# Optimization experiments

Measured on AMD Instinct MI355X. Metric: run time of the kernel, lower is better.

The kernel has to match this reference:

```python
import jax, jax.numpy as jnp
import numpy as np
from jax import lax

K = 3          # kernel size
PAD = 1        # (K-1)//2
CIN = 256
COUT = 64
NSPLIT = CIN // COUT  # 4
EPS = 1e-5


def _conv2d(x, w, b):
    # x [B,C,H,W], w [O,I,K,K], b [O]
    y = lax.conv_general_dilated(x, w, (1, 1), [(PAD, PAD), (PAD, PAD)],
                                 dimension_numbers=("NCHW", "OIHW", "NCHW"))
    return y + b[None, :, None, None]


def _bilinear_sample(img, py, px):
    # img [C,H,W]; py,px [K2,H,W] absolute sample coords; zero outside borders
    H, W = img.shape[1], img.shape[2]
    y0 = jnp.floor(py)
    x0 = jnp.floor(px)
    wy1 = py - y0
    wx1 = px - x0
    wy0 = 1.0 - wy1
    wx0 = 1.0 - wx1

    def gather(yc, xc):
        valid = (yc >= 0) & (yc <= H - 1) & (xc >= 0) & (xc <= W - 1)
        yi = jnp.clip(yc, 0, H - 1).astype(jnp.int32)
        xi = jnp.clip(xc, 0, W - 1).astype(jnp.int32)
        v = img[:, yi, xi]  # [C,K2,H,W]
        return v * valid.astype(img.dtype)[None]

    return (gather(y0, x0) * (wy0 * wx0)[None]
            + gather(y0, x0 + 1.0) * (wy0 * wx1)[None]
            + gather(y0 + 1.0, x0) * (wy1 * wx0)[None]
            + gather(y0 + 1.0, x0 + 1.0) * (wy1 * wx1)[None])


def _deform_conv(x, offsets, w, b):
    # x [B,C,H,W]; offsets [B,2*K2,H,W] (torchvision layout: per kernel pt (dy,dx));
    # w [O,C,K,K]; b [O]
    B, C, H, W = x.shape
    K2 = K * K
    off = offsets.reshape(B, K2, 2, H, W)
    kh = jnp.arange(K, dtype=x.dtype)
    base_y = (jnp.arange(H, dtype=x.dtype)[None, :, None]
              + (kh[:, None] - PAD).repeat(K).reshape(K2, 1, 1))  # h + kh - pad
    base_x = (jnp.arange(W, dtype=x.dtype)[None, None, :]
              + jnp.tile(kh - PAD, K).reshape(K2, 1, 1))          # w + kw - pad
    py = base_y + off[:, :, 0]  # [B,K2,H,W]
    px = base_x + off[:, :, 1]
    sampled = jax.vmap(_bilinear_sample)(x, py, px)  # [B,C,K2,H,W]
    out = jnp.einsum("bckhw,ock->bohw", sampled, w.reshape(w.shape[0], C, K2))
    return out + b[None, :, None, None]


def setup_inputs() -> dict:
    key = jax.random.key(0)
    ks = jax.random.split(key, 10)
    B, H, W = 8, 64, 64
    x = jax.random.normal(ks[0], (B, CIN, H, W), dtype=jnp.float32)
    bn_gamma = jax.random.normal(ks[1], (CIN,), dtype=jnp.float32) * 0.1 + 1.0
    bn_beta = jax.random.normal(ks[2], (CIN,), dtype=jnp.float32) * 0.1
    bn_mean = jax.random.normal(ks[3], (CIN,), dtype=jnp.float32) * 0.1
    bn_var = jax.random.uniform(ks[4], (CIN,), dtype=jnp.float32, minval=0.5, maxval=1.5)
    offset_w = jax.random.normal(ks[5], (NSPLIT, 2 * K * K, CIN, K, K), dtype=jnp.float32) * 0.02
    offset_b = jax.random.normal(ks[6], (NSPLIT, 2 * K * K), dtype=jnp.float32) * 0.02
    dconv_w = jax.random.normal(ks[7], (NSPLIT, COUT, COUT, K, K), dtype=jnp.float32) * 0.04
    dconv_b = jax.random.normal(ks[8], (NSPLIT, COUT), dtype=jnp.float32) * 0.02
    return {"x": x, "bn_gamma": bn_gamma, "bn_beta": bn_beta, "bn_mean": bn_mean,
            "bn_var": bn_var, "offset_w": offset_w, "offset_b": offset_b,
            "dconv_w": dconv_w, "dconv_b": dconv_b}


def reference(x, bn_gamma, bn_beta, bn_mean, bn_var, offset_w, offset_b, dconv_w, dconv_b):
    # BN (eval-mode running stats) + ReLU
    inv = lax.rsqrt(bn_var + EPS)
    h = jax.nn.relu((x - bn_mean[None, :, None, None]) * (bn_gamma * inv)[None, :, None, None]
                    + bn_beta[None, :, None, None])
    out = None
    for i in range(NSPLIT):
        offsets = _conv2d(h, offset_w[i], offset_b[i])               # [B,2K2,H,W]
        x_i = h[:, i * COUT:(i + 1) * COUT]                          # [B,COUT,H,W]
        y_i = _deform_conv(x_i, offsets, dconv_w[i], dconv_b[i])
        out = y_i if out is None else out + y_i
    return out
```

## Files before the change

kernel.cpp:

```cpp
#include <hip/hip_runtime.h>

#define KK 3
#define CIN 256
#define COUT 64
#define NSPLIT 4
#define BB 8
#define HH 64
#define WW 64
#define K2 9
#define OC 18
#define EPS 1e-5f

typedef __attribute__((ext_vector_type(8))) short bf16x8;
typedef __attribute__((ext_vector_type(4))) float f32x4;
typedef __attribute__((ext_vector_type(4))) unsigned int u32x4;

#define WS_SCALE 0
#define WS_BIAS  256
#define WS_BSUM  512
#define WS_HBF   1024
#define HBF_FLOATS (BB*HH*WW*CIN/2)
#define WS_OFFS  (WS_HBF + HBF_FLOATS)
#define OFFS_SIZE (BB*72*HH*WW)
#define WS_WDT   (WS_OFFS + OFFS_SIZE)
#define WS_WOB   (WS_WDT + NSPLIT*K2*COUT*COUT/2)
#define WOB_ELEMS (K2*80*CIN)

__device__ __host__ inline unsigned short f2bf(float f) {
    unsigned int u = __builtin_bit_cast(unsigned int, f);
    unsigned int r = (u + 0x7fffu + ((u >> 16) & 1u)) >> 16;
    return (unsigned short)r;
}
__device__ inline float bf2f(unsigned short u) {
    return __builtin_bit_cast(float, (unsigned int)u << 16);
}

__global__ void prep_kernel(const float* __restrict__ g, const float* __restrict__ be,
                            const float* __restrict__ mn, const float* __restrict__ vr,
                            const float* __restrict__ db, float* __restrict__ ws) {
    int t = threadIdx.x;
    if (t < CIN) {
        float inv = 1.0f / sqrtf(vr[t] + EPS);
        float sc = g[t] * inv;
        ws[WS_SCALE + t] = sc;
        ws[WS_BIAS + t]  = be[t] - mn[t] * sc;
    }
    if (t < COUT) {
        float s = 0.f;
        for (int i = 0; i < NSPLIT; i++) s += db[i * COUT + t];
        ws[WS_BSUM + t] = s;
    }
}

__global__ void wtrans_kernel(const float* __restrict__ dw, const float* __restrict__ ow,
                              float* __restrict__ ws) {
    int tid = blockIdx.x * blockDim.x + threadIdx.x;
    if (tid < NSPLIT * K2 * COUT * COUT) {
        int cin = tid & 63;
        int o = (tid >> 6) & 63;
        int k = (tid / 4096) % 9;
        int s = tid / 36864;
        ((unsigned short*)(ws + WS_WDT))[tid] = f2bf(dw[((s * COUT + o) * COUT + cin) * 9 + k]);
    }
    if (tid < WOB_ELEMS) {
        int cin = tid & 255;
        int sc = (tid >> 8) % 80;
        int k = tid / 20480;
        unsigned short v = 0;
        if (sc < 72) {
            int s = sc / 18, c = sc % 18;
            v = f2bf(ow[((s * OC + c) * CIN + cin) * 9 + k]);
        }
        ((unsigned short*)(ws + WS_WOB))[tid] = v;
    }
}

__global__ __launch_bounds__(256) void bn_transpose_kernel(const float* __restrict__ x,
                                                           const float* __restrict__ scb,
                                                           unsigned short* __restrict__ hbf) {
    __shared__ float tile[64 * 65];
    int cg = blockIdx.x;
    int y  = blockIdx.y;
    int b  = blockIdx.z;
    int lane = threadIdx.x & 63;
    int grp  = threadIdx.x >> 6;
    #pragma unroll
    for (int i = 0; i < 16; i++) {
        int cl = grp * 16 + i;
        int c  = cg * 64 + cl;
        float v = x[((b * CIN + c) * HH + y) * WW + lane];
        float h = fmaxf(fmaf(v, scb[c], scb[256 + c]), 0.f);
        tile[cl * 65 + lane] = h;
    }
    __syncthreads();
    int cpair = threadIdx.x & 31;
    int pxg   = threadIdx.x >> 5;
    #pragma unroll
    for (int i = 0; i < 8; i++) {
        int px = pxg * 8 + i;
        unsigned int u0 = f2bf(tile[(cpair * 2) * 65 + px]);
        unsigned int u1 = f2bf(tile[(cpair * 2 + 1) * 65 + px]);
        *(unsigned int*)&hbf[((size_t)(b * HH + y) * WW + px) * CIN + cg * 64 + cpair * 2] =
            u0 | (u1 << 16);
    }
}

__global__ __launch_bounds__(256) void offconv_kernel(const unsigned short* __restrict__ hbf,
                                                      const float* __restrict__ offb,
                                                      const unsigned short* __restrict__ woB,
                                                      float* __restrict__ offs_out) {
    __shared__ unsigned short wlds[80 * 264];
    int tid = threadIdx.x;
    int bid = blockIdx.x + 64 * blockIdx.y;
    int b = bid & 7;
    int y = bid >> 3;
    int w  = tid >> 6;
    int l  = tid & 63;
    int lm = l & 15, lk = l >> 4;
    int px = w * 16 + lm;

    f32x4 acc[5];
    #pragma unroll
    for (int nt = 0; nt < 5; nt++) {
        int sc = nt * 16 + lm;
        float ob = (sc < 72) ? offb[sc] : 0.f;
        acc[nt] = (f32x4){ob, ob, ob, ob};
    }
    const unsigned short* hb = hbf + (size_t)b * HH * WW * CIN;
    const bf16x8 zero = {};

    for (int k = 0; k < 9; k++) {
        int dy = k / 3 - 1, dx = k % 3 - 1;
        int ry = y + dy;
        if ((unsigned)ry >= (unsigned)HH) continue;
        __syncthreads();
        const unsigned short* src = woB + (size_t)k * 80 * 256;
        #pragma unroll
        for (int t = 0; t < 10; t++) {
            int idx = tid + t * 256;
            int sc = idx >> 5;
            int co = (idx & 31) * 8;
            *(bf16x8*)&wlds[sc * 264 + co] = *(const bf16x8*)&src[sc * 256 + co];
        }
        __syncthreads();

        int rx = px + dx;
        bool vx = (unsigned)rx < (unsigned)WW;
        const unsigned short* arow = hb + ((size_t)ry * WW + rx) * CIN + lk * 8;
        #pragma unroll
        for (int kt = 0; kt < 8; kt++) {
            bf16x8 a = vx ? *(const bf16x8*)(arow + kt * 32) : zero;
            #pragma unroll
            for (int nt = 0; nt < 5; nt++) {
                bf16x8 bb = *(const bf16x8*)&wlds[(nt * 16 + lm) * 264 + kt * 32 + lk * 8];
                acc[nt] = __builtin_amdgcn_mfma_f32_16x16x32_bf16(a, bb, acc[nt], 0, 0, 0);
            }
        }
    }

    #pragma unroll
    for (int nt = 0; nt < 5; nt++) {
        int sc = nt * 16 + lm;
        if (sc < 72) {
            float4 v = {acc[nt][0], acc[nt][1], acc[nt][2], acc[nt][3]};
            *(float4*)&offs_out[((size_t)(b * 72 + sc) * HH + y) * WW + w * 16 + lk * 4] = v;
        }
    }
}

#define RGN 14848
__global__ __launch_bounds__(512) void deform_kernel(const unsigned short* __restrict__ hbf,
                                                     const float* __restrict__ offp,
                                                     const unsigned short* __restrict__ wdT,
                                                     const float* __restrict__ bsum,
                                                     float* __restrict__ out) {
    __shared__ __align__(16) char lds[2][RGN];

    int tid = threadIdx.x;
    int bid = blockIdx.x + 128 * blockIdx.y;
    int b  = bid & 7;
    int r  = bid >> 3;
    int y  = r >> 1;
    int xh = r & 1;

    int h  = tid >> 8;
    int t8 = tid & 255;
    int l  = tid & 63;
    int w4 = t8 >> 6;
    int wm = w4 >> 1;
    int wn = w4 & 1;
    int lm = l & 15;
    int lk = l >> 4;
    int pA = (t8 >> 2) & 31;
    int cA = t8 & 3;
    int gp = t8 >> 3;
    int ch = (t8 & 7) * 8;

    unsigned short* vbufS = (unsigned short*)&lds[h][0];
    unsigned short* wbufS = (unsigned short*)&lds[h][4608];
    int*            tblI  = (int*)&lds[h][13824];

    f32x4 acc[2];
    #pragma unroll
    for (int j = 0; j < 2; j++) {
        float bs = h ? 0.f : bsum[(wn * 2 + j) * 16 + lm];
        acc[j] = (f32x4){bs, bs, bs, bs};
    }

    const unsigned short* hb = hbf + (size_t)b * HH * WW * CIN;
    const float* offbase = offp + ((size_t)(b * 72 + 2 * h * 18) * HH + y) * WW + xh * 32 + pA;

    float offy_c = offbase[0];
    float offx_c = offbase[HH * WW];

    for (int it = 0; it < 2 * K2; ++it) {
        int sl = it >= K2;
        int s  = 2 * h + sl;
        int k  = it - sl * K2;

        float offy_n = 0.f, offx_n = 0.f;
        if (it + 1 < 2 * K2) {
            int sl2 = (it + 1) >= K2;
            int k2  = (it + 1) - sl2 * K2;
            const float* oa = offbase + (size_t)(sl2 * 18 + 2 * k2) * (HH * WW);
            offy_n = oa[0];
            offx_n = oa[HH * WW];
        }

        const unsigned short* wsrc = wdT + (size_t)((s * 9 + k) * 64) * 64;
        bf16x8 wr0 = *(const bf16x8*)(wsrc + t8 * 16);
        bf16x8 wr1 = *(const bf16x8*)(wsrc + t8 * 16 + 8);

        {
            int dy = k / 3 - 1, dx = k % 3 - 1;
            float py  = (float)(y + dy) + offy_c;
            float px_ = (float)(xh * 32 + pA + dx) + offx_c;
            float y0f = floorf(py), x0f = floorf(px_);
            float wy1 = py - y0f, wx1 = px_ - x0f;
            int yt = (int)y0f + (cA >> 1);
            int xt = (int)x0f + (cA & 1);
            float wt = ((cA >> 1) ? wy1 : 1.f - wy1) * ((cA & 1) ? wx1 : 1.f - wx1);
            bool valid = (yt >= 0) && (yt < HH) && (xt >= 0) && (xt < WW);
            wt = valid ? wt : 0.f;
            int yi = min(max(yt, 0), HH - 1);
            int xi = min(max(xt, 0), WW - 1);
            int2 e = {yi * WW + xi, __builtin_bit_cast(int, wt)};
            *(int2*)&tblI[(pA * 4 + cA) * 2] = e;
        }
        __syncthreads();

        float v0[8];
        #pragma unroll
        for (int j = 0; j < 8; j++) v0[j] = 0.f;
        #pragma unroll
        for (int c = 0; c < 4; c++) {
            int2 t0 = *(const int2*)&tblI[(gp * 4 + c) * 2];
            const unsigned short* sp0 = hb + (size_t)t0.x * CIN + s * COUT + ch;
            bf16x8 d0 = *(const bf16x8*)sp0;
            float w0 = __builtin_bit_cast(float, t0.y);
            #pragma unroll
            for (int j = 0; j < 8; j++) {
                v0[j] = fmaf(w0, bf2f((unsigned short)d0[j]), v0[j]);
            }
        }
        {
            u32x4 q0;
            #pragma unroll
            for (int j = 0; j < 4; j++) {
                q0[j] = (unsigned)f2bf(v0[2 * j]) | ((unsigned)f2bf(v0[2 * j + 1]) << 16);
            }
            *(u32x4*)&vbufS[gp * 72 + ch] = q0;
        }
        {
            int wo = t8 >> 2, wpart = t8 & 3;
            *(bf16x8*)(&wbufS[wo * 72 + wpart * 16])     = wr0;
            *(bf16x8*)(&wbufS[wo * 72 + wpart * 16 + 8]) = wr1;
        }
        __syncthreads();

        #pragma unroll
        for (int ks = 0; ks < 2; ks++) {
            bf16x8 a = *(const bf16x8*)(&vbufS[(wm * 16 + lm) * 72 + ks * 32 + lk * 8]);
            #pragma unroll
            for (int j = 0; j < 2; j++) {
                bf16x8 bb = *(const bf16x8*)(&wbufS[((wn * 2 + j) * 16 + lm) * 72 + ks * 32 + lk * 8]);
                acc[j] = __builtin_amdgcn_mfma_f32_16x16x32_bf16(a, bb, acc[j], 0, 0, 0);
            }
        }

        offy_c = offy_n;
        offx_c = offx_n;
    }

    __syncthreads();
    float* outT = (float*)&lds[h][0];
    #pragma unroll
    for (int j = 0; j < 2; j++) {
        *(f32x4*)(&outT[((wn * 2 + j) * 16 + lm) * 36 + wm * 16 + lk * 4]) = acc[j];
    }
    __syncthreads();
    {
        const float* o0 = (const float*)&lds[0][0];
        const float* o1 = (const float*)&lds[1][0];
        int o = tid >> 3, xq = (tid & 7) * 4;
        float4 a = *(const float4*)(&o0[o * 36 + xq]);
        float4 c = *(const float4*)(&o1[o * 36 + xq]);
        float4 rr = {a.x + c.x, a.y + c.y, a.z + c.z, a.w + c.w};
        *(float4*)(out + (((size_t)(b * COUT + o)) * HH + y) * WW + xh * 32 + xq) = rr;
    }
}

extern "C" void kernel_launch(void* const* d_in, const int* in_sizes, int n_in,
                              void* d_out, int out_size, void* d_ws, size_t ws_size,
                              hipStream_t stream) {
    const float* x        = (const float*)d_in[0];
    const float* bn_gamma = (const float*)d_in[1];
    const float* bn_beta  = (const float*)d_in[2];
    const float* bn_mean  = (const float*)d_in[3];
    const float* bn_var   = (const float*)d_in[4];
    const float* offset_w = (const float*)d_in[5];
    const float* offset_b = (const float*)d_in[6];
    const float* dconv_w  = (const float*)d_in[7];
    const float* dconv_b  = (const float*)d_in[8];
    float* out = (float*)d_out;
    float* ws  = (float*)d_ws;

    unsigned short* hbf = (unsigned short*)(ws + WS_HBF);

    prep_kernel<<<1, 256, 0, stream>>>(bn_gamma, bn_beta, bn_mean, bn_var, dconv_b, ws);
    wtrans_kernel<<<(WOB_ELEMS + 255) / 256, 256, 0, stream>>>(dconv_w, offset_w, ws);
    bn_transpose_kernel<<<dim3(4, 64, 8), 256, 0, stream>>>(x, ws, hbf);
    offconv_kernel<<<dim3(64, 8), 256, 0, stream>>>(hbf, offset_b,
                                                    (const unsigned short*)(ws + WS_WOB),
                                                    ws + WS_OFFS);
    deform_kernel<<<dim3(128, 8), 512, 0, stream>>>(hbf, ws + WS_OFFS,
                                                    (const unsigned short*)(ws + WS_WDT),
                                                    ws + WS_BSUM, out);
}
```

Before: 101.8 us.

## Apply bilinear weights after MFMA instead of blending gathered values

The deform kernel now stores all four raw bilinear corner samples in swizzled LDS and runs one MFMA per corner. It then scales each partial result by that corner's per-pixel bilinear weight and accumulates in fp32. This drops the per-thread blend and bf16 repack and avoids LDS bank conflicts through XOR swizzling, at the cost of four times the MFMA work and more LDS. The prep kernel is also folded into the weight-transpose kernel to save a launch.

```diff
diff --git a/kernel.cpp b/kernel.cpp
--- a/kernel.cpp
+++ b/kernel.cpp
@@ -35,26 +35,26 @@
     return __builtin_bit_cast(float, (unsigned int)u << 16);
 }
 
-__global__ void prep_kernel(const float* __restrict__ g, const float* __restrict__ be,
-                            const float* __restrict__ mn, const float* __restrict__ vr,
-                            const float* __restrict__ db, float* __restrict__ ws) {
-    int t = threadIdx.x;
-    if (t < CIN) {
-        float inv = 1.0f / sqrtf(vr[t] + EPS);
-        float sc = g[t] * inv;
-        ws[WS_SCALE + t] = sc;
-        ws[WS_BIAS + t]  = be[t] - mn[t] * sc;
-    }
-    if (t < COUT) {
-        float s = 0.f;
-        for (int i = 0; i < NSPLIT; i++) s += db[i * COUT + t];
-        ws[WS_BSUM + t] = s;
-    }
-}
-
 __global__ void wtrans_kernel(const float* __restrict__ dw, const float* __restrict__ ow,
+                              const float* __restrict__ g, const float* __restrict__ be,
+                              const float* __restrict__ mn, const float* __restrict__ vr,
+                              const float* __restrict__ db,
                               float* __restrict__ ws) {
     int tid = blockIdx.x * blockDim.x + threadIdx.x;
+    if (blockIdx.x == 0) {
+        int t = threadIdx.x;
+        if (t < CIN) {
+            float inv = 1.0f / sqrtf(vr[t] + EPS);
+            float sc = g[t] * inv;
+            ws[WS_SCALE + t] = sc;
+            ws[WS_BIAS + t]  = be[t] - mn[t] * sc;
+        }
+        if (t < COUT) {
+            float s = 0.f;
+            for (int i = 0; i < NSPLIT; i++) s += db[i * COUT + t];
+            ws[WS_BSUM + t] = s;
+        }
+    }
     if (tid < NSPLIT * K2 * COUT * COUT) {
         int cin = tid & 63;
         int o = (tid >> 6) & 63;
@@ -168,12 +168,12 @@
     }
 }
 
-#define RGN 14848
-__global__ __launch_bounds__(512) void deform_kernel(const unsigned short* __restrict__ hbf,
-                                                     const float* __restrict__ offp,
-                                                     const unsigned short* __restrict__ wdT,
-                                                     const float* __restrict__ bsum,
-                                                     float* __restrict__ out) {
+#define RGN 25600
+__global__ __launch_bounds__(512, 4) void deform_kernel(const unsigned short* __restrict__ hbf,
+                                                        const float* __restrict__ offp,
+                                                        const unsigned short* __restrict__ wdT,
+                                                        const float* __restrict__ bsum,
+                                                        float* __restrict__ out) {
     __shared__ __align__(16) char lds[2][RGN];
 
     int tid = threadIdx.x;
@@ -191,14 +191,14 @@
     int wn = w4 & 1;
     int lm = l & 15;
     int lk = l >> 4;
-    int pA = (t8 >> 2) & 31;
+    int pA = t8 >> 2;
     int cA = t8 & 3;
     int gp = t8 >> 3;
-    int ch = (t8 & 7) * 8;
-
-    unsigned short* vbufS = (unsigned short*)&lds[h][0];
-    unsigned short* wbufS = (unsigned short*)&lds[h][4608];
-    int*            tblI  = (int*)&lds[h][13824];
+    int ch8 = (t8 & 7) * 8;
+
+    char* half = lds[h];
+    int*   tblI = (int*)(half + 24576);
+    float* wtF  = (float*)(half + 25088);
 
     f32x4 acc[2];
     #pragma unroll
@@ -208,10 +208,14 @@
     }
 
     const unsigned short* hb = hbf + (size_t)b * HH * WW * CIN;
-    const float* offbase = offp + ((size_t)(b * 72 + 2 * h * 18) * HH + y) * WW + xh * 32 + pA;
-
-    float offy_c = offbase[0];
-    float offx_c = offbase[HH * WW];
+    bool tblOwner = (t8 < 128);
+    const float* offbase = offp + ((size_t)(b * 72 + 2 * h * 18) * HH + y) * WW + xh * 32 + (pA & 31);
+
+    float offy_c = 0.f, offx_c = 0.f;
+    if (tblOwner) {
+        offy_c = offbase[0];
+        offx_c = offbase[HH * WW];
+    }
 
     for (int it = 0; it < 2 * K2; ++it) {
         int sl = it >= K2;
@@ -219,7 +223,7 @@
         int k  = it - sl * K2;
 
         float offy_n = 0.f, offx_n = 0.f;
-        if (it + 1 < 2 * K2) {
+        if (tblOwner && it + 1 < 2 * K2) {
             int sl2 = (it + 1) >= K2;
             int k2  = (it + 1) - sl2 * K2;
             const float* oa = offbase + (size_t)(sl2 * 18 + 2 * k2) * (HH * WW);
@@ -231,7 +235,7 @@
         bf16x8 wr0 = *(const bf16x8*)(wsrc + t8 * 16);
         bf16x8 wr1 = *(const bf16x8*)(wsrc + t8 * 16 + 8);
 
-        {
+        if (tblOwner) {
             int dy = k / 3 - 1, dx = k % 3 - 1;
             float py  = (float)(y + dy) + offy_c;
             float px_ = (float)(xh * 32 + pA + dx) + offx_c;
@@ -244,47 +248,74 @@
             wt = valid ? wt : 0.f;
             int yi = min(max(yt, 0), HH - 1);
             int xi = min(max(xt, 0), WW - 1);
-            int2 e = {yi * WW + xi, __builtin_bit_cast(int, wt)};
-            *(int2*)&tblI[(pA * 4 + cA) * 2] = e;
+            tblI[pA * 4 + cA] = yi * WW + xi;
+            wtF [pA * 4 + cA] = wt;
         }
         __syncthreads();
 
-        float v0[8];
+        {
+            int4 pos = *(const int4*)&tblI[gp * 4];
+            const unsigned short* sbase = hb + s * COUT + ch8;
+            bf16x8 d0 = *(const bf16x8*)(sbase + (size_t)pos.x * CIN);
+            bf16x8 d1 = *(const bf16x8*)(sbase + (size_t)pos.y * CIN);
+            bf16x8 d2 = *(const bf16x8*)(sbase + (size_t)pos.z * CIN);
+            bf16x8 d3 = *(const bf16x8*)(sbase + (size_t)pos.w * CIN);
+            char* vb = half + gp * 128 + ((ch8 * 2) ^ ((gp & 7) << 4));
+            *(bf16x8*)(vb)         = d0;
+            *(bf16x8*)(vb + 4096)  = d1;
+            *(bf16x8*)(vb + 8192)  = d2;
+            *(bf16x8*)(vb + 12288) = d3;
+        }
+        f32x4 wtv[4];
         #pragma unroll
-        for (int j = 0; j < 8; j++) v0[j] = 0.f;
-        #pragma unroll
-        for (int c = 0; c < 4; c++) {
-            int2 t0 = *(const int2*)&tblI[(gp * 4 + c) * 2];
-            const unsigned short* sp0 = hb + (size_t)t0.x * CIN + s * COUT + ch;
-            bf16x8 d0 = *(const bf16x8*)sp0;
-            float w0 = __builtin_bit_cast(float, t0.y);
+        for (int jj = 0; jj < 4; jj++)
+            wtv[jj] = *(const f32x4*)&wtF[(wm * 16 + lk * 4 + jj) * 4];
+        {
+            int wo = t8 >> 2, wq = t8 & 3;
+            char* wb = half + 16384 + wo * 128;
+            int sw = (wo & 7) << 4;
+            *(bf16x8*)(wb + ((wq * 32) ^ sw))      = wr0;
+            *(bf16x8*)(wb + ((wq * 32 + 16) ^ sw)) = wr1;
+        }
+        __syncthreads();
+
+        {
+            bf16x8 bbf[2][2];
             #pragma unroll
-            for (int j = 0; j < 8; j++) {
-                v0[j] = fmaf(w0, bf2f((unsigned short)d0[j]), v0[j]);
+            for (int ks = 0; ks < 2; ks++) {
+                #pragma unroll
+                for (int j = 0; j < 2; j++) {
+                    int row = (wn * 2 + j) * 16 + lm;
+                    bbf[ks][j] = *(const bf16x8*)(half + 16384 + row * 128 +
+                                                  ((ks * 64 + lk * 16) ^ ((lm & 7) << 4)));
+                }
             }
-        }
-        {
-            u32x4 q0;
+            int arow = wm * 16 + lm;
+            int aswz = (lm & 7) << 4;
             #pragma unroll
-            for (int j = 0; j < 4; j++) {
-                q0[j] = (unsigned)f2bf(v0[2 * j]) | ((unsigned)f2bf(v0[2 * j + 1]) << 16);
-            }
-            *(u32x4*)&vbufS[gp * 72 + ch] = q0;
-        }
-        {
-            int wo = t8 >> 2, wpart = t8 & 3;
-            *(bf16x8*)(&wbufS[wo * 72 + wpart * 16])     = wr0;
-            *(bf16x8*)(&wbufS[wo * 72 + wpart * 16 + 8]) = wr1;
-        }
-        __syncthreads();
-
-        #pragma unroll
-        for (int ks = 0; ks < 2; ks++) {
-            bf16x8 a = *(const bf16x8*)(&vbufS[(wm * 16 + lm) * 72 + ks * 32 + lk * 8]);
-            #pragma unroll
-            for (int j = 0; j < 2; j++) {
-                bf16x8 bb = *(const bf16x8*)(&wbufS[((wn * 2 + j) * 16 + lm) * 72 + ks * 32 + lk * 8]);
-                acc[j] = __builtin_amdgcn_mfma_f32_16x16x32_bf16(a, bb, acc[j], 0, 0, 0);
+            for (int pass = 0; pass < 2; pass++) {
+                f32x4 t0[2] = {(f32x4){0,0,0,0}, (f32x4){0,0,0,0}};
+                f32x4 t1[2] = {(f32x4){0,0,0,0}, (f32x4){0,0,0,0}};
+                #pragma unroll
+                for (int ks = 0; ks < 2; ks++) {
+                    bf16x8 a0 = *(const bf16x8*)(half + ((pass * 2 + 0) * 32 + arow) * 128 +
+                                                 ((ks * 64 + lk * 16) ^ aswz));
+                    bf16x8 a1 = *(const bf16x8*)(half + ((pass * 2 + 1) * 32 + arow) * 128 +
+                                                 ((ks * 64 + lk * 16) ^ aswz));
+                    #pragma unroll
+                    for (int j = 0; j < 2; j++) {
+                        t0[j] = __builtin_amdgcn_mfma_f32_16x16x32_bf16(a0, bbf[ks][j], t0[j], 0, 0, 0);
+                        t1[j] = __builtin_amdgcn_mfma_f32_16x16x32_bf16(a1, bbf[ks][j], t1[j], 0, 0, 0);
+                    }
+                }
+                #pragma unroll
+                for (int j = 0; j < 2; j++) {
+                    #pragma unroll
+                    for (int reg = 0; reg < 4; reg++) {
+                        acc[j][reg] = fmaf(wtv[reg][pass * 2],     t0[j][reg], acc[j][reg]);
+                        acc[j][reg] = fmaf(wtv[reg][pass * 2 + 1], t1[j][reg], acc[j][reg]);
+                    }
+                }
             }
         }
 
@@ -293,15 +324,15 @@
     }
 
     __syncthreads();
-    float* outT = (float*)&lds[h][0];
+    float* outT = (float*)half;
     #pragma unroll
     for (int j = 0; j < 2; j++) {
         *(f32x4*)(&outT[((wn * 2 + j) * 16 + lm) * 36 + wm * 16 + lk * 4]) = acc[j];
     }
     __syncthreads();
     {
-        const float* o0 = (const float*)&lds[0][0];
-        const float* o1 = (const float*)&lds[1][0];
+        const float* o0 = (const float*)lds[0];
+        const float* o1 = (const float*)lds[1];
         int o = tid >> 3, xq = (tid & 7) * 4;
         float4 a = *(const float4*)(&o0[o * 36 + xq]);
         float4 c = *(const float4*)(&o1[o * 36 + xq]);
@@ -327,8 +358,9 @@
 
     unsigned short* hbf = (unsigned short*)(ws + WS_HBF);
 
-    prep_kernel<<<1, 256, 0, stream>>>(bn_gamma, bn_beta, bn_mean, bn_var, dconv_b, ws);
-    wtrans_kernel<<<(WOB_ELEMS + 255) / 256, 256, 0, stream>>>(dconv_w, offset_w, ws);
+    wtrans_kernel<<<(WOB_ELEMS + 255) / 256, 256, 0, stream>>>(dconv_w, offset_w,
+                                                               bn_gamma, bn_beta, bn_mean,
+                                                               bn_var, dconv_b, ws);
     bn_transpose_kernel<<<dim3(4, 64, 8), 256, 0, stream>>>(x, ws, hbf);
     offconv_kernel<<<dim3(64, 8), 256, 0, stream>>>(hbf, offset_b,
                                                     (const unsigned short*)(ws + WS_WOB),
```

Measured after the change: 108.5 us. 1.07x slower.

## Build deform MFMA operands in registers, drop LDS staging and fold prep kernel

Applied to the files above, without the earlier changes.

In the deform kernel, each lane now computes its own bilinear sample coordinates and gathers the input channels it needs directly into MFMA A-operand registers. Weight B-operands are also loaded straight from global memory, so the per-iteration LDS tables, operand buffers and their two barriers are gone. The prep kernel is merged into the weight-transpose kernel to save one launch, and launch bounds now request 4 waves per SIMD. The trade-off is redundant coordinate math and gathers across the lanes and waves that share pixels, plus heavier direct global weight loads.

```diff
diff --git a/kernel.cpp b/kernel.cpp
--- a/kernel.cpp
+++ b/kernel.cpp
@@ -13,7 +13,6 @@
 
 typedef __attribute__((ext_vector_type(8))) short bf16x8;
 typedef __attribute__((ext_vector_type(4))) float f32x4;
-typedef __attribute__((ext_vector_type(4))) unsigned int u32x4;
 
 #define WS_SCALE 0
 #define WS_BIAS  256
@@ -35,26 +34,26 @@
     return __builtin_bit_cast(float, (unsigned int)u << 16);
 }
 
-__global__ void prep_kernel(const float* __restrict__ g, const float* __restrict__ be,
-                            const float* __restrict__ mn, const float* __restrict__ vr,
-                            const float* __restrict__ db, float* __restrict__ ws) {
-    int t = threadIdx.x;
-    if (t < CIN) {
-        float inv = 1.0f / sqrtf(vr[t] + EPS);
-        float sc = g[t] * inv;
-        ws[WS_SCALE + t] = sc;
-        ws[WS_BIAS + t]  = be[t] - mn[t] * sc;
-    }
-    if (t < COUT) {
-        float s = 0.f;
-        for (int i = 0; i < NSPLIT; i++) s += db[i * COUT + t];
-        ws[WS_BSUM + t] = s;
-    }
-}
-
 __global__ void wtrans_kernel(const float* __restrict__ dw, const float* __restrict__ ow,
+                              const float* __restrict__ g, const float* __restrict__ be,
+                              const float* __restrict__ mn, const float* __restrict__ vr,
+                              const float* __restrict__ db,
                               float* __restrict__ ws) {
     int tid = blockIdx.x * blockDim.x + threadIdx.x;
+    if (blockIdx.x == 0) {
+        int t = threadIdx.x;
+        if (t < CIN) {
+            float inv = 1.0f / sqrtf(vr[t] + EPS);
+            float sc = g[t] * inv;
+            ws[WS_SCALE + t] = sc;
+            ws[WS_BIAS + t]  = be[t] - mn[t] * sc;
+        }
+        if (t < COUT) {
+            float s = 0.f;
+            for (int i = 0; i < NSPLIT; i++) s += db[i * COUT + t];
+            ws[WS_BSUM + t] = s;
+        }
+    }
     if (tid < NSPLIT * K2 * COUT * COUT) {
         int cin = tid & 63;
         int o = (tid >> 6) & 63;
@@ -168,13 +167,12 @@
     }
 }
 
-#define RGN 14848
-__global__ __launch_bounds__(512) void deform_kernel(const unsigned short* __restrict__ hbf,
-                                                     const float* __restrict__ offp,
-                                                     const unsigned short* __restrict__ wdT,
-                                                     const float* __restrict__ bsum,
-                                                     float* __restrict__ out) {
-    __shared__ __align__(16) char lds[2][RGN];
+__global__ __launch_bounds__(512, 4) void deform_kernel(const unsigned short* __restrict__ hbf,
+                                                        const float* __restrict__ offp,
+                                                        const unsigned short* __restrict__ wdT,
+                                                        const float* __restrict__ bsum,
+                                                        float* __restrict__ out) {
+    __shared__ float outT[2][64 * 36];
 
     int tid = threadIdx.x;
     int bid = blockIdx.x + 128 * blockIdx.y;
@@ -183,35 +181,29 @@
     int y  = r >> 1;
     int xh = r & 1;
 
-    int h  = tid >> 8;
-    int t8 = tid & 255;
-    int l  = tid & 63;
-    int w4 = t8 >> 6;
+    int w  = tid >> 6;
+    int h  = w >> 2;
+    int w4 = w & 3;
     int wm = w4 >> 1;
     int wn = w4 & 1;
+    int l  = tid & 63;
     int lm = l & 15;
     int lk = l >> 4;
-    int pA = (t8 >> 2) & 31;
-    int cA = t8 & 3;
-    int gp = t8 >> 3;
-    int ch = (t8 & 7) * 8;
-
-    unsigned short* vbufS = (unsigned short*)&lds[h][0];
-    unsigned short* wbufS = (unsigned short*)&lds[h][4608];
-    int*            tblI  = (int*)&lds[h][13824];
+    int p  = xh * 32 + wm * 16 + lm;
 
     f32x4 acc[2];
     #pragma unroll
-    for (int j = 0; j < 2; j++) {
-        float bs = h ? 0.f : bsum[(wn * 2 + j) * 16 + lm];
-        acc[j] = (f32x4){bs, bs, bs, bs};
+    for (int nt = 0; nt < 2; nt++) {
+        float bs = h ? 0.f : bsum[wn * 32 + nt * 16 + lm];
+        acc[nt] = (f32x4){bs, bs, bs, bs};
     }
 
     const unsigned short* hb = hbf + (size_t)b * HH * WW * CIN;
-    const float* offbase = offp + ((size_t)(b * 72 + 2 * h * 18) * HH + y) * WW + xh * 32 + pA;
-
-    float offy_c = offbase[0];
-    float offx_c = offbase[HH * WW];
+    const float* obp = offp + (size_t)b * 72 * (HH * WW) + y * WW + p;
+
+    int sc0 = 2 * h * 18;
+    float offy_c = obp[(size_t)sc0 * (HH * WW)];
+    float offx_c = obp[(size_t)(sc0 + 1) * (HH * WW)];
 
     for (int it = 0; it < 2 * K2; ++it) {
         int sl = it >= K2;
@@ -222,89 +214,75 @@
         if (it + 1 < 2 * K2) {
             int sl2 = (it + 1) >= K2;
             int k2  = (it + 1) - sl2 * K2;
-            const float* oa = offbase + (size_t)(sl2 * 18 + 2 * k2) * (HH * WW);
-            offy_n = oa[0];
-            offx_n = oa[HH * WW];
-        }
-
-        const unsigned short* wsrc = wdT + (size_t)((s * 9 + k) * 64) * 64;
-        bf16x8 wr0 = *(const bf16x8*)(wsrc + t8 * 16);
-        bf16x8 wr1 = *(const bf16x8*)(wsrc + t8 * 16 + 8);
-
-        {
-            int dy = k / 3 - 1, dx = k % 3 - 1;
-            float py  = (float)(y + dy) + offy_c;
-            float px_ = (float)(xh * 32 + pA + dx) + offx_c;
-            float y0f = floorf(py), x0f = floorf(px_);
-            float wy1 = py - y0f, wx1 = px_ - x0f;
-            int yt = (int)y0f + (cA >> 1);
-            int xt = (int)x0f + (cA & 1);
-            float wt = ((cA >> 1) ? wy1 : 1.f - wy1) * ((cA & 1) ? wx1 : 1.f - wx1);
+            int sc2 = (2 * h + sl2) * 18 + 2 * k2;
+            offy_n = obp[(size_t)sc2 * (HH * WW)];
+            offx_n = obp[(size_t)(sc2 + 1) * (HH * WW)];
+        }
+
+        int dy = k / 3 - 1, dx = k % 3 - 1;
+        float py  = (float)(y + dy) + offy_c;
+        float pxx = (float)(p + dx) + offx_c;
+        float y0f = floorf(py), x0f = floorf(pxx);
+        float wy1 = py - y0f, wx1 = pxx - x0f;
+        int y0 = (int)y0f, x0 = (int)x0f;
+        int pos[4]; float wt[4];
+        #pragma unroll
+        for (int c = 0; c < 4; c++) {
+            int yt = y0 + (c >> 1), xt = x0 + (c & 1);
+            float w_ = ((c >> 1) ? wy1 : 1.f - wy1) * ((c & 1) ? wx1 : 1.f - wx1);
             bool valid = (yt >= 0) && (yt < HH) && (xt >= 0) && (xt < WW);
-            wt = valid ? wt : 0.f;
-            int yi = min(max(yt, 0), HH - 1);
-            int xi = min(max(xt, 0), WW - 1);
-            int2 e = {yi * WW + xi, __builtin_bit_cast(int, wt)};
-            *(int2*)&tblI[(pA * 4 + cA) * 2] = e;
-        }
-        __syncthreads();
-
-        float v0[8];
-        #pragma unroll
-        for (int j = 0; j < 8; j++) v0[j] = 0.f;
+            wt[c] = valid ? w_ : 0.f;
+            pos[c] = min(max(yt, 0), HH - 1) * WW + min(max(xt, 0), WW - 1);
+        }
+
+        const unsigned short* sb = hb + s * COUT + lk * 8;
+        float v0[8], v1[8];
+        #pragma unroll
+        for (int j = 0; j < 8; j++) { v0[j] = 0.f; v1[j] = 0.f; }
         #pragma unroll
         for (int c = 0; c < 4; c++) {
-            int2 t0 = *(const int2*)&tblI[(gp * 4 + c) * 2];
-            const unsigned short* sp0 = hb + (size_t)t0.x * CIN + s * COUT + ch;
-            bf16x8 d0 = *(const bf16x8*)sp0;
-            float w0 = __builtin_bit_cast(float, t0.y);
+            const unsigned short* spc = sb + (size_t)pos[c] * CIN;
+            bf16x8 d0 = *(const bf16x8*)(spc);
+            bf16x8 d1 = *(const bf16x8*)(spc + 32);
+            float w_ = wt[c];
             #pragma unroll
             for (int j = 0; j < 8; j++) {
-                v0[j] = fmaf(w0, bf2f((unsigned short)d0[j]), v0[j]);
+                v0[j] = fmaf(w_, bf2f((unsigned short)d0[j]), v0[j]);
+                v1[j] = fmaf(w_, bf2f((unsigned short)d1[j]), v1[j]);
             }
         }
-        {
-            u32x4 q0;
-            #pragma unroll
-            for (int j = 0; j < 4; j++) {
-                q0[j] = (unsigned)f2bf(v0[2 * j]) | ((unsigned)f2bf(v0[2 * j + 1]) << 16);
-            }
-            *(u32x4*)&vbufS[gp * 72 + ch] = q0;
-        }
-        {
-            int wo = t8 >> 2, wpart = t8 & 3;
-            *(bf16x8*)(&wbufS[wo * 72 + wpart * 16])     = wr0;
-            *(bf16x8*)(&wbufS[wo * 72 + wpart * 16 + 8]) = wr1;
-        }
-        __syncthreads();
-
-        #pragma unroll
-        for (int ks = 0; ks < 2; ks++) {
-            bf16x8 a = *(const bf16x8*)(&vbufS[(wm * 16 + lm) * 72 + ks * 32 + lk * 8]);
-            #pragma unroll
-            for (int j = 0; j < 2; j++) {
-                bf16x8 bb = *(const bf16x8*)(&wbufS[((wn * 2 + j) * 16 + lm) * 72 + ks * 32 + lk * 8]);
-                acc[j] = __builtin_amdgcn_mfma_f32_16x16x32_bf16(a, bb, acc[j], 0, 0, 0);
-            }
-        }
+        bf16x8 a0, a1;
+        #pragma unroll
+        for (int j = 0; j < 8; j++) {
+            a0[j] = (short)f2bf(v0[j]);
+            a1[j] = (short)f2bf(v1[j]);
+        }
+
+        const unsigned short* wsrc = wdT + (size_t)((s * 9 + k) * 64) * 64
+                                   + (size_t)(wn * 32 + lm) * 64 + lk * 8;
+        bf16x8 b00 = *(const bf16x8*)(wsrc);
+        bf16x8 b01 = *(const bf16x8*)(wsrc + 32);
+        bf16x8 b10 = *(const bf16x8*)(wsrc + 1024);
+        bf16x8 b11 = *(const bf16x8*)(wsrc + 1024 + 32);
+
+        acc[0] = __builtin_amdgcn_mfma_f32_16x16x32_bf16(a0, b00, acc[0], 0, 0, 0);
+        acc[0] = __builtin_amdgcn_mfma_f32_16x16x32_bf16(a1, b01, acc[0], 0, 0, 0);
+        acc[1] = __builtin_amdgcn_mfma_f32_16x16x32_bf16(a0, b10, acc[1], 0, 0, 0);
+        acc[1] = __builtin_amdgcn_mfma_f32_16x16x32_bf16(a1, b11, acc[1], 0, 0, 0);
 
         offy_c = offy_n;
         offx_c = offx_n;
     }
 
-    __syncthreads();
-    float* outT = (float*)&lds[h][0];
-    #pragma unroll
-    for (int j = 0; j < 2; j++) {
-        *(f32x4*)(&outT[((wn * 2 + j) * 16 + lm) * 36 + wm * 16 + lk * 4]) = acc[j];
+    #pragma unroll
+    for (int nt = 0; nt < 2; nt++) {
+        *(f32x4*)(&outT[h][(wn * 32 + nt * 16 + lm) * 36 + wm * 16 + lk * 4]) = acc[nt];
     }
     __syncthreads();
     {
-        const float* o0 = (const float*)&lds[0][0];
-        const float* o1 = (const float*)&lds[1][0];
         int o = tid >> 3, xq = (tid & 7) * 4;
-        float4 a = *(const float4*)(&o0[o * 36 + xq]);
-        float4 c = *(const float4*)(&o1[o * 36 + xq]);
+        float4 a = *(const float4*)(&outT[0][o * 36 + xq]);
+        float4 c = *(const float4*)(&outT[1][o * 36 + xq]);
         float4 rr = {a.x + c.x, a.y + c.y, a.z + c.z, a.w + c.w};
         *(float4*)(out + (((size_t)(b * COUT + o)) * HH + y) * WW + xh * 32 + xq) = rr;
     }
@@ -327,8 +305,9 @@
 
     unsigned short* hbf = (unsigned short*)(ws + WS_HBF);
 
-    prep_kernel<<<1, 256, 0, stream>>>(bn_gamma, bn_beta, bn_mean, bn_var, dconv_b, ws);
-    wtrans_kernel<<<(WOB_ELEMS + 255) / 256, 256, 0, stream>>>(dconv_w, offset_w, ws);
+    wtrans_kernel<<<(WOB_ELEMS + 255) / 256, 256, 0, stream>>>(dconv_w, offset_w,
+                                                               bn_gamma, bn_beta, bn_mean,
+                                                               bn_var, dconv_b, ws);
     bn_transpose_kernel<<<dim3(4, 64, 8), 256, 0, stream>>>(x, ws, hbf);
     offconv_kernel<<<dim3(64, 8), 256, 0, stream>>>(hbf, offset_b,
                                                     (const unsigned short*)(ws + WS_WOB),
```

After: 230.2 us. 2.26x slower.
